# Kernel optimization log

Measured on AMD Instinct MI355X. Metric: run time of the kernel, lower is better.

## Reference

```python
import jax, jax.numpy as jnp
import numpy as np

EPS_BN = 1e-5
EPS_NORM = 1e-12


def setup_inputs() -> dict:
    dim, mid, k = 128, 32, 3
    b, h, w = 8, 128, 128
    key = jax.random.key(0)
    ks = jax.random.split(key, 16)
    s = 0.05
    return {
        "x": jax.random.normal(ks[0], (b, dim, h, w), jnp.float32),
        "w_spatial_in": jax.random.normal(ks[1], (dim, dim), jnp.float32) * s,
        "w_dw_spatial": jax.random.normal(ks[2], (dim, 1, k), jnp.float32) * s,
        "w_spatial_out": jax.random.normal(ks[3], (dim, dim), jnp.float32) * s,
        "w_ch_in": jax.random.normal(ks[4], (dim, dim), jnp.float32) * s,
        "w_ch_dw": jax.random.normal(ks[5], (dim, 1, k), jnp.float32) * s,
        "w_ch_out": jax.random.normal(ks[6], (dim, dim), jnp.float32) * s,
        "w_mlp1": jax.random.normal(ks[7], (mid, dim), jnp.float32) * s,
        "b_mlp1": jax.random.normal(ks[8], (mid,), jnp.float32) * s,
        "w_mlp2": jax.random.normal(ks[9], (dim, mid), jnp.float32) * s,
        "b_mlp2": jax.random.normal(ks[10], (dim,), jnp.float32) * s,
        "diff_weight": jnp.float32(1.0),
        "bn_gamma": jnp.ones((dim,), jnp.float32),
        "bn_beta": jnp.zeros((dim,), jnp.float32),
        "w_out_proj": jax.random.normal(ks[11], (dim, dim), jnp.float32) * s,
    }


def _dwconv1d(seq, wk):
    # seq: [b, c, L], wk: [c, 1, k] depthwise, 'same' padding
    c = seq.shape[1]
    k = wk.shape[-1]
    return jax.lax.conv_general_dilated(
        seq, wk, window_strides=(1,), padding=[(k // 2, k // 2)],
        dimension_numbers=("NCH", "OIH", "NCH"), feature_group_count=c)


def _ocs_forward(x, w_spatial_in, w_dw_spatial, w_spatial_out,
                 w_ch_in, w_ch_dw, w_ch_out,
                 w_mlp1, b_mlp1, w_mlp2, b_mlp2,
                 diff_weight, bn_gamma, bn_beta, w_out_proj):
    b, c, h, w = x.shape
    L = h * w
    alpha = beta = eta = 1.0

    # ---- scan indices (4 orders) ----
    idx_row = jnp.arange(L)
    gy, gx = jnp.meshgrid(jnp.arange(h), jnp.arange(w), indexing="ij")
    idx_col = (gx * h + gy).reshape(-1)
    orders = [idx_row, idx_row[::-1], idx_col, idx_col[::-1]]

    x_seq0 = x.reshape(b, c, L).transpose(0, 2, 1)  # [b, L, c]

    def scan(idx):
        s = x_seq0[:, idx]                                   # gather   [b,L,c]
        s = jnp.einsum("blc,oc->blo", s, w_spatial_in)       # linear
        s = _dwconv1d(s.transpose(0, 2, 1), w_dw_spatial)    # dw conv  [b,c,L]
        s = jnp.einsum("bcl,oc->blo", s, w_spatial_out)      # linear   [b,L,c]
        s = s.at[:, idx].set(s[:, jnp.arange(L)]) if False else s[:, jnp.argsort(idx)]  # scatter back (inverse perm)
        return s.transpose(0, 2, 1).reshape(b, c, h, w)

    y_sp = (scan(orders[0]) + scan(orders[1]) + scan(orders[2]) + scan(orders[3])) * 0.25

    # ---- channel branch ----
    seq = x.reshape(b, c, L)
    seq = jnp.einsum("oc,bcl->bol", w_ch_in, seq)
    seq = _dwconv1d(seq, w_ch_dw)
    seq = jnp.einsum("oc,bcl->bol", w_ch_out, seq)
    gap = x.mean((2, 3))                                     # [b,c]
    gap = gap / jnp.maximum(jnp.linalg.norm(gap, axis=1, keepdims=True), EPS_NORM)
    m = jnp.einsum("bi,bj->bij", gap, gap)                   # [b,c,c]
    seq_agg = jnp.einsum("bij,bjl->bil", m, seq)             # [b,c,L]
    h1 = jax.nn.silu(jnp.einsum("mc,bcl->bml", w_mlp1, seq_agg) + b_mlp1[None, :, None])
    y_ch = (jnp.einsum("cm,bml->bcl", w_mlp2, h1) + b_mlp2[None, :, None]).reshape(b, c, h, w)

    # ---- difference branch (reflect-pad 4-neighbor abs diff) ----
    p = jnp.pad(x, ((0, 0), (0, 0), (1, 1), (1, 1)), mode="reflect")
    cx = p[:, :, 1:-1, 1:-1]
    diff = (jnp.abs(cx - p[:, :, 1:-1, :-2]) + jnp.abs(cx - p[:, :, 1:-1, 2:])
            + jnp.abs(cx - p[:, :, :-2, 1:-1]) + jnp.abs(cx - p[:, :, 2:, 1:-1])) * 0.25
    y_diff = x + diff_weight * diff

    # ---- combine, 1x1 proj, batchnorm (training-mode batch stats) ----
    y = alpha * y_sp + beta * y_ch + eta * y_diff
    y = jnp.einsum("oc,bchw->bohw", w_out_proj, y)
    mu = y.mean((0, 2, 3))
    var = y.var((0, 2, 3))
    y = (y - mu[None, :, None, None]) * jax.lax.rsqrt(var + EPS_BN)[None, :, None, None]
    y = y * bn_gamma[None, :, None, None] + bn_beta[None, :, None, None]
    return y


def reference(x, w_spatial_in, w_dw_spatial, w_spatial_out, w_ch_in, w_ch_dw,
              w_ch_out, w_mlp1, b_mlp1, w_mlp2, b_mlp2, diff_weight,
              bn_gamma, bn_beta, w_out_proj):
    return _ocs_forward(x, w_spatial_in, w_dw_spatial, w_spatial_out,
                        w_ch_in, w_ch_dw, w_ch_out, w_mlp1, b_mlp1,
                        w_mlp2, b_mlp2, diff_weight, bn_gamma, bn_beta,
                        w_out_proj)
```

## Files before the change

### kernel.cpp

```cpp
#include <hip/hip_runtime.h>
#include <hip/hip_bf16.h>

#define C 128
#define L 16384
#define B 8
#define MID 32
#define NBL (B * L)

typedef unsigned short ushort_t;
typedef __attribute__((ext_vector_type(8))) short s8v;
typedef __attribute__((ext_vector_type(4))) float f4v;

__device__ __forceinline__ unsigned short f2bf(float f) {
    union { float f; unsigned int u; } a; a.f = f;
    unsigned int u = a.u;
    return (unsigned short)((u + 0x7fffu + ((u >> 16) & 1u)) >> 16);
}

__device__ __forceinline__ void load8(const ushort_t* p, float* f) {
    uint4 u = *(const uint4*)p;
    f[0] = __uint_as_float(u.x << 16); f[1] = __uint_as_float(u.x & 0xffff0000u);
    f[2] = __uint_as_float(u.y << 16); f[3] = __uint_as_float(u.y & 0xffff0000u);
    f[4] = __uint_as_float(u.z << 16); f[5] = __uint_as_float(u.z & 0xffff0000u);
    f[6] = __uint_as_float(u.w << 16); f[7] = __uint_as_float(u.w & 0xffff0000u);
}

__device__ __forceinline__ void zero8(float* f) {
#pragma unroll
    for (int j = 0; j < 8; j++) f[j] = 0.f;
}

__device__ __forceinline__ void store8(ushort_t* p, const float* f) {
    union { ushort_t h[8]; uint4 q; } u;
#pragma unroll
    for (int j = 0; j < 8; j++) u.h[j] = f2bf(f[j]);
    *(uint4*)p = u.q;
}

__device__ __forceinline__ void ld8f(const float* p, float* f) {
    float4 a = *(const float4*)p;
    float4 b = *(const float4*)(p + 4);
    f[0] = a.x; f[1] = a.y; f[2] = a.z; f[3] = a.w;
    f[4] = b.x; f[5] = b.y; f[6] = b.z; f[7] = b.w;
}

__global__ __launch_bounds__(256) void k_cvt(const float* __restrict__ x,
                                             ushort_t* __restrict__ xb,
                                             float* __restrict__ gap) {
    __shared__ float xs[64][129];
    const int bid = blockIdx.x;
    const int b = bid >> 8;
    const int l0 = (bid & 255) * 64;
    const int tid = threadIdx.x;
    const int c = tid >> 1, h = tid & 1;
    const float* src = x + ((size_t)(b * C + c)) * L + l0 + h * 32;
    float s = 0.f;
#pragma unroll
    for (int j = 0; j < 8; j++) {
        float4 v = *(const float4*)(src + j * 4);
        s += (v.x + v.y) + (v.z + v.w);
        int lb = h * 32 + j * 4;
        xs[lb + 0][c] = v.x; xs[lb + 1][c] = v.y;
        xs[lb + 2][c] = v.z; xs[lb + 3][c] = v.w;
    }
    s += __shfl_xor(s, 1);
    if (h == 0) atomicAdd(&gap[b * C + c], s);
    __syncthreads();
    const int l = tid & 63, quarter = tid >> 6, cb = quarter * 32;
    union { ushort_t hh[32]; uint4 q[4]; } u;
#pragma unroll
    for (int k = 0; k < 32; k++) u.hh[k] = f2bf(xs[l][cb + k]);
    uint4* dst = (uint4*)(xb + ((size_t)(b * L + l0 + l)) * C + cb);
#pragma unroll
    for (int k = 0; k < 4; k++) dst[k] = u.q[k];
}

__global__ __launch_bounds__(128) void k_prep_b(const float* __restrict__ gap,
                                                const float* __restrict__ w1,
                                                const float* __restrict__ Wco,
                                                float* __restrict__ a,
                                                float* __restrict__ gw) {
    int b = blockIdx.x, c = threadIdx.x;
    __shared__ float gl[C];
    __shared__ float red[C];
    float v = gap[b * C + c] * (1.f / (float)L);
    red[c] = v * v;
    __syncthreads();
    for (int w = 64; w > 0; w >>= 1) {
        if (c < w) red[c] += red[c + w];
        __syncthreads();
    }
    float nrm = fmaxf(sqrtf(red[0]), 1e-12f);
    float gc = v / nrm;
    gl[c] = gc;
    __syncthreads();
    if (c < MID) {
        float s = 0.f;
        for (int k = 0; k < C; k++) s = fmaf(w1[c * C + k], gl[k], s);
        a[b * MID + c] = s;
    }
    {
        float s = 0.f;
        for (int k = 0; k < C; k++) s = fmaf(gl[k], Wco[k * C + c], s);
        gw[b * C + c] = s;
    }
}

__global__ __launch_bounds__(128) void k_prep_w(const float* __restrict__ Win,
                                                const float* __restrict__ Wci,
                                                const float* __restrict__ Wproj,
                                                const float* __restrict__ Wout,
                                                const float* __restrict__ w2,
                                                const float* __restrict__ b2,
                                                const float* __restrict__ wds,
                                                const float* __restrict__ wcd,
                                                ushort_t* __restrict__ Wio,
                                                ushort_t* __restrict__ Wcat,
                                                float* __restrict__ bp,
                                                float* __restrict__ kwS,
                                                float* __restrict__ kw1,
                                                float* __restrict__ kd0,
                                                float* __restrict__ kd1,
                                                float* __restrict__ kd2) {
    int o = blockIdx.x, c = threadIdx.x;
    __shared__ float pr[C];
    pr[c] = Wproj[o * C + c];
    __syncthreads();
    Wio[o * C + c] = f2bf(Win[o * C + c]);
    Wio[(C + o) * C + c] = f2bf(Wci[o * C + c]);
    float s = 0.f;
    for (int k = 0; k < C; k++) s = fmaf(pr[k], Wout[k * C + c], s);
    Wcat[o * 288 + c] = f2bf(s);
    Wcat[o * 288 + 128 + c] = f2bf(pr[c]);
    if (c < MID) {
        float s2 = 0.f;
        for (int k = 0; k < C; k++) s2 = fmaf(pr[k], w2[k * MID + c], s2);
        Wcat[o * 288 + 256 + c] = f2bf(s2);
    }
    if (c == 0) {
        float s3 = 0.f;
        for (int k = 0; k < C; k++) s3 = fmaf(pr[k], b2[k], s3);
        bp[o] = s3;
    }
    if (o == 0) {
        kwS[c] = 0.25f * (wds[3 * c] + wds[3 * c + 2]);
        kw1[c] = wds[3 * c + 1];
        kd0[c] = wcd[3 * c];
        kd1[c] = wcd[3 * c + 1];
        kd2[c] = wcd[3 * c + 2];
    }
}

__global__ __launch_bounds__(512, 1) void k_gemm1(const ushort_t* __restrict__ xb,
                                                  const ushort_t* __restrict__ Wio,
                                                  ushort_t* __restrict__ tu) {
    __shared__ ushort_t wl[128 * 136];
    const int tid = threadIdx.x;
    const int bid = blockIdx.x;
    const int b = bid >> 8;
    const int ms = (bid >> 7) & 1;
    const int lt = bid & 127;
    {
        int row = tid >> 2, qq = tid & 3;
        const uint4* s4 = (const uint4*)(Wio + (ms * C + row) * C + qq * 32);
        uint4* d4 = (uint4*)(wl + row * 136 + qq * 32);
        d4[0] = s4[0]; d4[1] = s4[1]; d4[2] = s4[2]; d4[3] = s4[3];
    }
    __syncthreads();
    const int wave = tid >> 6, lane = tid & 63;
    const int l0 = lt * 128 + wave * 16;
    const int n = lane & 15, q = lane >> 4;
    const ushort_t* brow = xb + ((size_t)(b * L + l0 + n)) * C + q * 8;
    s8v bfrag[4];
#pragma unroll
    for (int ks = 0; ks < 4; ks++) bfrag[ks] = *(const s8v*)(brow + ks * 32);
    f4v acc[8];
#pragma unroll
    for (int i = 0; i < 8; i++) acc[i] = (f4v){0.f, 0.f, 0.f, 0.f};
#pragma unroll
    for (int ks = 0; ks < 4; ks++) {
#pragma unroll
        for (int mt = 0; mt < 8; mt++) {
            s8v af = *(const s8v*)(wl + (mt * 16 + n) * 136 + ks * 32 + q * 8);
            acc[mt] = __builtin_amdgcn_mfma_f32_16x16x32_bf16(af, bfrag[ks], acc[mt], 0, 0, 0);
        }
    }
    ushort_t* orow = tu + ((size_t)(b * L + l0 + n)) * 256 + ms * C + q * 4;
#pragma unroll
    for (int mt = 0; mt < 8; mt++) {
        union { ushort_t h[4]; uint2 q2; } u;
#pragma unroll
        for (int i = 0; i < 4; i++) u.h[i] = f2bf(acc[mt][i]);
        *(uint2*)(orow + mt * 16) = u.q2;
    }
}

__global__ __launch_bounds__(256) void k_mid(const ushort_t* __restrict__ tu,
                                             const ushort_t* __restrict__ xb,
                                             const float* __restrict__ kwS,
                                             const float* __restrict__ kw1,
                                             const float* __restrict__ kd0,
                                             const float* __restrict__ kd1,
                                             const float* __restrict__ kd2,
                                             const float* __restrict__ gw,
                                             const float* __restrict__ a,
                                             const float* __restrict__ b1,
                                             const float* __restrict__ pdw,
                                             ushort_t* __restrict__ Kb) {
    const int tid = threadIdx.x;
    const int cc = tid & 15, p = tid >> 4;
    const int bid = blockIdx.x;
    const int b = bid >> 10;
    const int l = (bid & 1023) * 16 + p;
    const int y = l >> 7, xg = l & 127;
    const int c0 = cc * 8;
    const size_t rb = (size_t)b * L;

    const int rL = (l > 0) ? (l - 1) : -1;
    const int rR = (l < L - 1) ? (l + 1) : -1;
    const int rU = (y > 0) ? (l - 128) : ((xg > 0) ? (16256 + xg - 1) : -1);
    const int rD = (y < 127) ? (l + 128) : ((xg < 127) ? (xg + 1) : -1);
    const int sL = (xg > 0) ? (l - 1) : (l + 1);
    const int sR = (xg < 127) ? (l + 1) : (l - 1);
    const int sU = (y > 0) ? (l - 128) : (l + 128);
    const int sD = (y < 127) ? (l + 128) : (l - 128);

    float tC[8], tLe[8], tRi[8], tUp[8], tDo[8];
    load8(tu + (rb + l) * 256 + c0, tC);
    if (rL >= 0) load8(tu + (rb + rL) * 256 + c0, tLe); else zero8(tLe);
    if (rR >= 0) load8(tu + (rb + rR) * 256 + c0, tRi); else zero8(tRi);
    if (rU >= 0) load8(tu + (rb + rU) * 256 + c0, tUp); else zero8(tUp);
    if (rD >= 0) load8(tu + (rb + rD) * 256 + c0, tDo); else zero8(tDo);

    float uC[8], uL8[8], uR8[8];
    load8(tu + (rb + l) * 256 + 128 + c0, uC);
    if (rL >= 0) load8(tu + (rb + rL) * 256 + 128 + c0, uL8); else zero8(uL8);
    if (rR >= 0) load8(tu + (rb + rR) * 256 + 128 + c0, uR8); else zero8(uR8);

    float xC[8], xL8[8], xR8[8], xU8[8], xD8[8];
    load8(xb + (rb + l) * C + c0, xC);
    load8(xb + (rb + sL) * C + c0, xL8);
    load8(xb + (rb + sR) * C + c0, xR8);
    load8(xb + (rb + sU) * C + c0, xU8);
    load8(xb + (rb + sD) * C + c0, xD8);

    float kS[8], k1[8], d0[8], d1[8], d2[8], gv[8];
    ld8f(kwS + c0, kS); ld8f(kw1 + c0, k1);
    ld8f(kd0 + c0, d0); ld8f(kd1 + c0, d1); ld8f(kd2 + c0, d2);
    ld8f(gw + b * C + c0, gv);
    const float dwt = pdw[0] * 0.25f;

    float ct[8], yd[8];
    float s1 = 0.f;
#pragma unroll
    for (int j = 0; j < 8; j++) {
        ct[j] = kS[j] * ((tLe[j] + tRi[j]) + (tUp[j] + tDo[j])) + k1[j] * tC[j];
        float vv = d0[j] * uL8[j] + d1[j] * uC[j] + d2[j] * uR8[j];
        s1 = fmaf(gv[j], vv, s1);
        float cen = xC[j];
        float d = fabsf(cen - xL8[j]) + fabsf(cen - xR8[j]) +
                  fabsf(cen - xU8[j]) + fabsf(cen - xD8[j]);
        yd[j] = fmaf(dwt, d, cen);
    }
    s1 += __shfl_xor(s1, 1);
    s1 += __shfl_xor(s1, 2);
    s1 += __shfl_xor(s1, 4);
    s1 += __shfl_xor(s1, 8);

    ushort_t* kr = Kb + (rb + l) * 288;
    store8(kr + c0, ct);
    store8(kr + 128 + c0, yd);
    if (cc < 4) {
        float av[8], bv[8], sv[8];
        ld8f(a + b * MID + cc * 8, av);
        ld8f(b1 + cc * 8, bv);
#pragma unroll
        for (int j = 0; j < 8; j++) {
            float pre = fmaf(av[j], s1, bv[j]);
            sv[j] = pre / (1.f + __expf(-pre));
        }
        store8(kr + 256 + cc * 8, sv);
    }
}

__global__ __launch_bounds__(512, 1) void k_gemm2(const ushort_t* __restrict__ Kb,
                                                  const ushort_t* __restrict__ Wcat,
                                                  const float* __restrict__ bp,
                                                  float* __restrict__ outp) {
    __shared__ ushort_t wl[64 * 296];
    const int tid = threadIdx.x;
    const int bid = blockIdx.x;
    const int b = bid >> 8;
    const int ms = (bid >> 7) & 1;
    const int lt = bid & 127;
    for (int i = 0; i < 5; i++) {
        int idx = tid + i * 512;
        if (idx < 2304) {
            int row = idx / 36, col = idx - row * 36;
            *(uint4*)(wl + row * 296 + col * 8) =
                *(const uint4*)(Wcat + (ms * 64 + row) * 288 + col * 8);
        }
    }
    __syncthreads();
    const int wave = tid >> 6, lane = tid & 63;
    const int l0 = lt * 128 + wave * 16;
    const int n = lane & 15, q = lane >> 4;
    const ushort_t* brow = Kb + ((size_t)(b * L + l0 + n)) * 288 + q * 8;
    f4v acc[4];
#pragma unroll
    for (int i = 0; i < 4; i++) acc[i] = (f4v){0.f, 0.f, 0.f, 0.f};
#pragma unroll
    for (int ks = 0; ks < 9; ks++) {
        s8v bf_ = *(const s8v*)(brow + ks * 32);
#pragma unroll
        for (int mt = 0; mt < 4; mt++) {
            s8v af = *(const s8v*)(wl + (mt * 16 + n) * 296 + ks * 32 + q * 8);
            acc[mt] = __builtin_amdgcn_mfma_f32_16x16x32_bf16(af, bf_, acc[mt], 0, 0, 0);
        }
    }
#pragma unroll
    for (int mt = 0; mt < 4; mt++) {
        int o0 = ms * 64 + mt * 16 + q * 4;
        float4 bv = *(const float4*)(bp + o0);
        float ba[4] = {bv.x, bv.y, bv.z, bv.w};
#pragma unroll
        for (int i = 0; i < 4; i++) {
            outp[((size_t)(b * C + o0 + i)) * L + l0 + n] = acc[mt][i] + ba[i];
        }
    }
}

__global__ __launch_bounds__(256) void k_bnstats2(const float* __restrict__ outp,
                                                  float* __restrict__ stats) {
    const int bo = blockIdx.x;
    const int o = bo & (C - 1);
    const float4* p = (const float4*)(outp + (size_t)bo * L);
    float s = 0.f, sq = 0.f;
    for (int i = threadIdx.x; i < L / 4; i += 256) {
        float4 v = p[i];
        s += (v.x + v.y) + (v.z + v.w);
        sq += v.x * v.x + v.y * v.y + v.z * v.z + v.w * v.w;
    }
    __shared__ float rs[256], rq[256];
    rs[threadIdx.x] = s; rq[threadIdx.x] = sq;
    __syncthreads();
    for (int w = 128; w > 0; w >>= 1) {
        if (threadIdx.x < w) {
            rs[threadIdx.x] += rs[threadIdx.x + w];
            rq[threadIdx.x] += rq[threadIdx.x + w];
        }
        __syncthreads();
    }
    if (threadIdx.x == 0) {
        atomicAdd(&stats[o], rs[0]);
        atomicAdd(&stats[C + o], rq[0]);
    }
}

__global__ void k_bnfin(const float* __restrict__ stats, const float* __restrict__ gamma,
                        const float* __restrict__ beta, float* __restrict__ scsh) {
    int o = threadIdx.x;
    float n = (float)NBL;
    float mu = stats[o] / n;
    float var = stats[C + o] / n - mu * mu;
    float sc = gamma[o] * rsqrtf(var + 1e-5f);
    scsh[o] = sc;
    scsh[C + o] = fmaf(-mu, sc, beta[o]);
}

__global__ __launch_bounds__(256) void k_bnapply(float* __restrict__ outp,
                                                 const float* __restrict__ scsh) {
    int bo = blockIdx.x;
    int o = bo & (C - 1);
    float sc = scsh[o], sh = scsh[C + o];
    float4* p = (float4*)(outp + (size_t)bo * L);
    for (int i = threadIdx.x; i < L / 4; i += 256) {
        float4 v = p[i];
        v.x = fmaf(v.x, sc, sh);
        v.y = fmaf(v.y, sc, sh);
        v.z = fmaf(v.z, sc, sh);
        v.w = fmaf(v.w, sc, sh);
        p[i] = v;
    }
}

extern "C" void kernel_launch(void* const* d_in, const int* in_sizes, int n_in,
                              void* d_out, int out_size, void* d_ws, size_t ws_size,
                              hipStream_t stream) {
    const float* x = (const float*)d_in[0];
    const float* Win = (const float*)d_in[1];
    const float* wds = (const float*)d_in[2];
    const float* Wout = (const float*)d_in[3];
    const float* Wci = (const float*)d_in[4];
    const float* wcd = (const float*)d_in[5];
    const float* Wco = (const float*)d_in[6];
    const float* w1 = (const float*)d_in[7];
    const float* b1 = (const float*)d_in[8];
    const float* w2 = (const float*)d_in[9];
    const float* b2 = (const float*)d_in[10];
    const float* pdw = (const float*)d_in[11];
    const float* gamma = (const float*)d_in[12];
    const float* beta = (const float*)d_in[13];
    const float* Wproj = (const float*)d_in[14];

    char* wsb = (char*)d_ws;
    ushort_t* xb = (ushort_t*)wsb;
    ushort_t* tu = (ushort_t*)(wsb + 33554432);
    ushort_t* Kb = (ushort_t*)(wsb + 100663296);
    char* S = wsb + 176160768;
    float* gap  = (float*)(S + 0);
    float* stats= (float*)(S + 4096);
    float* scsh = (float*)(S + 5120);
    float* a    = (float*)(S + 6144);
    float* gw   = (float*)(S + 7168);
    float* bp   = (float*)(S + 11264);
    float* kwS  = (float*)(S + 11776);
    float* kw1  = (float*)(S + 12288);
    float* kd0  = (float*)(S + 12800);
    float* kd1  = (float*)(S + 13312);
    float* kd2  = (float*)(S + 13824);
    ushort_t* Wio  = (ushort_t*)(S + 14336);
    ushort_t* Wcat = (ushort_t*)(S + 79872);
    float* outp = (float*)d_out;

    hipMemsetAsync(S, 0, 5120, stream);
    k_cvt<<<2048, 256, 0, stream>>>(x, xb, gap);
    k_prep_b<<<8, 128, 0, stream>>>(gap, w1, Wco, a, gw);
    k_prep_w<<<128, 128, 0, stream>>>(Win, Wci, Wproj, Wout, w2, b2, wds, wcd,
                                      Wio, Wcat, bp, kwS, kw1, kd0, kd1, kd2);
    k_gemm1<<<2048, 512, 0, stream>>>(xb, Wio, tu);
    k_mid<<<8192, 256, 0, stream>>>(tu, xb, kwS, kw1, kd0, kd1, kd2, gw, a, b1, pdw, Kb);
    k_gemm2<<<2048, 512, 0, stream>>>(Kb, Wcat, bp, outp);
    k_bnstats2<<<1024, 256, 0, stream>>>(outp, stats);
    k_bnfin<<<1, 128, 0, stream>>>(stats, gamma, beta, scsh);
    k_bnapply<<<1024, 256, 0, stream>>>(outp, scsh);
}
```

Measured before the change: 313.9 us.

## Fuse mid stencil, second GEMM and BN stats into one kernel via LDS tile

The stencil/mix kernel now writes its 64-position K tile (bf16, 288 channels) into shared memory instead of a global Kb buffer. The same block then runs the second MFMA GEMM against Wcat, read straight from global, and accumulates per-channel sum and sum-of-squares with shuffles and atomics. This removes the Kb round trip through HBM and the separate stats pass over the output. The trade-off is more atomics, per-wave global loads of the weight fragments, and a heavier block, whose occupancy is set to 4 via launch bounds. bnapply is also split over twice as many blocks.

```diff
diff --git a/kernel.cpp b/kernel.cpp
--- a/kernel.cpp
+++ b/kernel.cpp
@@ -30,7 +30,7 @@
     for (int j = 0; j < 8; j++) f[j] = 0.f;
 }
 
-__device__ __forceinline__ void store8(ushort_t* p, const float* f) {
+__device__ __forceinline__ void store8_lds(ushort_t* p, const float* f) {
     union { ushort_t h[8]; uint4 q; } u;
 #pragma unroll
     for (int j = 0; j < 8; j++) u.h[j] = f2bf(f[j]);
@@ -195,165 +195,143 @@
     }
 }
 
-__global__ __launch_bounds__(256) void k_mid(const ushort_t* __restrict__ tu,
-                                             const ushort_t* __restrict__ xb,
-                                             const float* __restrict__ kwS,
-                                             const float* __restrict__ kw1,
-                                             const float* __restrict__ kd0,
-                                             const float* __restrict__ kd1,
-                                             const float* __restrict__ kd2,
-                                             const float* __restrict__ gw,
-                                             const float* __restrict__ a,
-                                             const float* __restrict__ b1,
-                                             const float* __restrict__ pdw,
-                                             ushort_t* __restrict__ Kb) {
+__global__ __launch_bounds__(256, 4) void k_fuse2(
+    const ushort_t* __restrict__ tu, const ushort_t* __restrict__ xb,
+    const float* __restrict__ kwS, const float* __restrict__ kw1,
+    const float* __restrict__ kd0, const float* __restrict__ kd1,
+    const float* __restrict__ kd2, const float* __restrict__ gw,
+    const float* __restrict__ a, const float* __restrict__ b1,
+    const float* __restrict__ pdw, const ushort_t* __restrict__ Wcat,
+    const float* __restrict__ bp, float* __restrict__ outp,
+    float* __restrict__ stats) {
+    __shared__ ushort_t Kl[64 * 296];
     const int tid = threadIdx.x;
-    const int cc = tid & 15, p = tid >> 4;
     const int bid = blockIdx.x;
-    const int b = bid >> 10;
-    const int l = (bid & 1023) * 16 + p;
-    const int y = l >> 7, xg = l & 127;
+    const int b = bid >> 8;
+    const int l0 = (bid & 255) * 64;
+    const size_t rb = (size_t)b * L;
+    const int cc = tid & 15, p16 = tid >> 4;
     const int c0 = cc * 8;
-    const size_t rb = (size_t)b * L;
-
-    const int rL = (l > 0) ? (l - 1) : -1;
-    const int rR = (l < L - 1) ? (l + 1) : -1;
-    const int rU = (y > 0) ? (l - 128) : ((xg > 0) ? (16256 + xg - 1) : -1);
-    const int rD = (y < 127) ? (l + 128) : ((xg < 127) ? (xg + 1) : -1);
-    const int sL = (xg > 0) ? (l - 1) : (l + 1);
-    const int sR = (xg < 127) ? (l + 1) : (l - 1);
-    const int sU = (y > 0) ? (l - 128) : (l + 128);
-    const int sD = (y < 127) ? (l + 128) : (l - 128);
-
-    float tC[8], tLe[8], tRi[8], tUp[8], tDo[8];
-    load8(tu + (rb + l) * 256 + c0, tC);
-    if (rL >= 0) load8(tu + (rb + rL) * 256 + c0, tLe); else zero8(tLe);
-    if (rR >= 0) load8(tu + (rb + rR) * 256 + c0, tRi); else zero8(tRi);
-    if (rU >= 0) load8(tu + (rb + rU) * 256 + c0, tUp); else zero8(tUp);
-    if (rD >= 0) load8(tu + (rb + rD) * 256 + c0, tDo); else zero8(tDo);
-
-    float uC[8], uL8[8], uR8[8];
-    load8(tu + (rb + l) * 256 + 128 + c0, uC);
-    if (rL >= 0) load8(tu + (rb + rL) * 256 + 128 + c0, uL8); else zero8(uL8);
-    if (rR >= 0) load8(tu + (rb + rR) * 256 + 128 + c0, uR8); else zero8(uR8);
-
-    float xC[8], xL8[8], xR8[8], xU8[8], xD8[8];
-    load8(xb + (rb + l) * C + c0, xC);
-    load8(xb + (rb + sL) * C + c0, xL8);
-    load8(xb + (rb + sR) * C + c0, xR8);
-    load8(xb + (rb + sU) * C + c0, xU8);
-    load8(xb + (rb + sD) * C + c0, xD8);
 
     float kS[8], k1[8], d0[8], d1[8], d2[8], gv[8];
     ld8f(kwS + c0, kS); ld8f(kw1 + c0, k1);
     ld8f(kd0 + c0, d0); ld8f(kd1 + c0, d1); ld8f(kd2 + c0, d2);
     ld8f(gw + b * C + c0, gv);
     const float dwt = pdw[0] * 0.25f;
-
-    float ct[8], yd[8];
-    float s1 = 0.f;
-#pragma unroll
-    for (int j = 0; j < 8; j++) {
-        ct[j] = kS[j] * ((tLe[j] + tRi[j]) + (tUp[j] + tDo[j])) + k1[j] * tC[j];
-        float vv = d0[j] * uL8[j] + d1[j] * uC[j] + d2[j] * uR8[j];
-        s1 = fmaf(gv[j], vv, s1);
-        float cen = xC[j];
-        float d = fabsf(cen - xL8[j]) + fabsf(cen - xR8[j]) +
-                  fabsf(cen - xU8[j]) + fabsf(cen - xD8[j]);
-        yd[j] = fmaf(dwt, d, cen);
-    }
-    s1 += __shfl_xor(s1, 1);
-    s1 += __shfl_xor(s1, 2);
-    s1 += __shfl_xor(s1, 4);
-    s1 += __shfl_xor(s1, 8);
-
-    ushort_t* kr = Kb + (rb + l) * 288;
-    store8(kr + c0, ct);
-    store8(kr + 128 + c0, yd);
-    if (cc < 4) {
-        float av[8], bv[8], sv[8];
-        ld8f(a + b * MID + cc * 8, av);
-        ld8f(b1 + cc * 8, bv);
+    float av[8], bv[8];
+    if (cc < 4) { ld8f(a + b * MID + cc * 8, av); ld8f(b1 + cc * 8, bv); }
+
+    for (int st = 0; st < 4; st++) {
+        const int p = st * 16 + p16;
+        const int l = l0 + p;
+        const int y = l >> 7, xg = l & 127;
+
+        const int rL = (l > 0) ? (l - 1) : -1;
+        const int rR = (l < L - 1) ? (l + 1) : -1;
+        const int rU = (y > 0) ? (l - 128) : ((xg > 0) ? (16256 + xg - 1) : -1);
+        const int rD = (y < 127) ? (l + 128) : ((xg < 127) ? (xg + 1) : -1);
+        const int sL = (xg > 0) ? (l - 1) : (l + 1);
+        const int sR = (xg < 127) ? (l + 1) : (l - 1);
+        const int sU = (y > 0) ? (l - 128) : (l + 128);
+        const int sD = (y < 127) ? (l + 128) : (l - 128);
+
+        float tC[8], tLe[8], tRi[8], tUp[8], tDo[8];
+        load8(tu + (rb + l) * 256 + c0, tC);
+        if (rL >= 0) load8(tu + (rb + rL) * 256 + c0, tLe); else zero8(tLe);
+        if (rR >= 0) load8(tu + (rb + rR) * 256 + c0, tRi); else zero8(tRi);
+        if (rU >= 0) load8(tu + (rb + rU) * 256 + c0, tUp); else zero8(tUp);
+        if (rD >= 0) load8(tu + (rb + rD) * 256 + c0, tDo); else zero8(tDo);
+
+        float uC[8], uL8[8], uR8[8];
+        load8(tu + (rb + l) * 256 + 128 + c0, uC);
+        if (rL >= 0) load8(tu + (rb + rL) * 256 + 128 + c0, uL8); else zero8(uL8);
+        if (rR >= 0) load8(tu + (rb + rR) * 256 + 128 + c0, uR8); else zero8(uR8);
+
+        float xC[8], xL8[8], xR8[8], xU8[8], xD8[8];
+        load8(xb + (rb + l) * C + c0, xC);
+        load8(xb + (rb + sL) * C + c0, xL8);
+        load8(xb + (rb + sR) * C + c0, xR8);
+        load8(xb + (rb + sU) * C + c0, xU8);
+        load8(xb + (rb + sD) * C + c0, xD8);
+
+        float ct[8], yd[8];
+        float s1 = 0.f;
 #pragma unroll
         for (int j = 0; j < 8; j++) {
-            float pre = fmaf(av[j], s1, bv[j]);
-            sv[j] = pre / (1.f + __expf(-pre));
+            ct[j] = kS[j] * ((tLe[j] + tRi[j]) + (tUp[j] + tDo[j])) + k1[j] * tC[j];
+            float vv = d0[j] * uL8[j] + d1[j] * uC[j] + d2[j] * uR8[j];
+            s1 = fmaf(gv[j], vv, s1);
+            float cen = xC[j];
+            float d = fabsf(cen - xL8[j]) + fabsf(cen - xR8[j]) +
+                      fabsf(cen - xU8[j]) + fabsf(cen - xD8[j]);
+            yd[j] = fmaf(dwt, d, cen);
         }
-        store8(kr + 256 + cc * 8, sv);
-    }
-}
-
-__global__ __launch_bounds__(512, 1) void k_gemm2(const ushort_t* __restrict__ Kb,
-                                                  const ushort_t* __restrict__ Wcat,
-                                                  const float* __restrict__ bp,
-                                                  float* __restrict__ outp) {
-    __shared__ ushort_t wl[64 * 296];
-    const int tid = threadIdx.x;
-    const int bid = blockIdx.x;
-    const int b = bid >> 8;
-    const int ms = (bid >> 7) & 1;
-    const int lt = bid & 127;
-    for (int i = 0; i < 5; i++) {
-        int idx = tid + i * 512;
-        if (idx < 2304) {
-            int row = idx / 36, col = idx - row * 36;
-            *(uint4*)(wl + row * 296 + col * 8) =
-                *(const uint4*)(Wcat + (ms * 64 + row) * 288 + col * 8);
+        s1 += __shfl_xor(s1, 1);
+        s1 += __shfl_xor(s1, 2);
+        s1 += __shfl_xor(s1, 4);
+        s1 += __shfl_xor(s1, 8);
+
+        ushort_t* kr = Kl + p * 296;
+        store8_lds(kr + c0, ct);
+        store8_lds(kr + 128 + c0, yd);
+        if (cc < 4) {
+            float sv[8];
+#pragma unroll
+            for (int j = 0; j < 8; j++) {
+                float pre = fmaf(av[j], s1, bv[j]);
+                sv[j] = pre / (1.f + __expf(-pre));
+            }
+            store8_lds(kr + 256 + cc * 8, sv);
         }
     }
     __syncthreads();
-    const int wave = tid >> 6, lane = tid & 63;
-    const int l0 = lt * 128 + wave * 16;
+
+    const int w = tid >> 6, lane = tid & 63;
     const int n = lane & 15, q = lane >> 4;
-    const ushort_t* brow = Kb + ((size_t)(b * L + l0 + n)) * 288 + q * 8;
-    f4v acc[4];
-#pragma unroll
-    for (int i = 0; i < 4; i++) acc[i] = (f4v){0.f, 0.f, 0.f, 0.f};
+    f4v acc[2][4];
+#pragma unroll
+    for (int m = 0; m < 2; m++)
+#pragma unroll
+        for (int t = 0; t < 4; t++) acc[m][t] = (f4v){0.f, 0.f, 0.f, 0.f};
+    const ushort_t* A0 = Wcat + ((w * 2 + 0) * 16 + n) * 288 + q * 8;
+    const ushort_t* A1 = Wcat + ((w * 2 + 1) * 16 + n) * 288 + q * 8;
 #pragma unroll
     for (int ks = 0; ks < 9; ks++) {
-        s8v bf_ = *(const s8v*)(brow + ks * 32);
-#pragma unroll
-        for (int mt = 0; mt < 4; mt++) {
-            s8v af = *(const s8v*)(wl + (mt * 16 + n) * 296 + ks * 32 + q * 8);
-            acc[mt] = __builtin_amdgcn_mfma_f32_16x16x32_bf16(af, bf_, acc[mt], 0, 0, 0);
+        s8v a0 = *(const s8v*)(A0 + ks * 32);
+        s8v a1 = *(const s8v*)(A1 + ks * 32);
+#pragma unroll
+        for (int t = 0; t < 4; t++) {
+            s8v bf_ = *(const s8v*)(Kl + (t * 16 + n) * 296 + ks * 32 + q * 8);
+            acc[0][t] = __builtin_amdgcn_mfma_f32_16x16x32_bf16(a0, bf_, acc[0][t], 0, 0, 0);
+            acc[1][t] = __builtin_amdgcn_mfma_f32_16x16x32_bf16(a1, bf_, acc[1][t], 0, 0, 0);
         }
     }
-#pragma unroll
-    for (int mt = 0; mt < 4; mt++) {
-        int o0 = ms * 64 + mt * 16 + q * 4;
-        float4 bv = *(const float4*)(bp + o0);
-        float ba[4] = {bv.x, bv.y, bv.z, bv.w};
+
+#pragma unroll
+    for (int mtl = 0; mtl < 2; mtl++) {
+        const int o0 = (w * 2 + mtl) * 16 + q * 4;
+        float4 bpv = *(const float4*)(bp + o0);
+        float ba[4] = {bpv.x, bpv.y, bpv.z, bpv.w};
 #pragma unroll
         for (int i = 0; i < 4; i++) {
-            outp[((size_t)(b * C + o0 + i)) * L + l0 + n] = acc[mt][i] + ba[i];
+            const int o = o0 + i;
+            float s = 0.f, sq = 0.f;
+#pragma unroll
+            for (int t = 0; t < 4; t++) {
+                float v = acc[mtl][t][i] + ba[i];
+                outp[((size_t)(b * C + o)) * L + l0 + t * 16 + n] = v;
+                s += v;
+                sq = fmaf(v, v, sq);
+            }
+            s += __shfl_xor(s, 1); s += __shfl_xor(s, 2);
+            s += __shfl_xor(s, 4); s += __shfl_xor(s, 8);
+            sq += __shfl_xor(sq, 1); sq += __shfl_xor(sq, 2);
+            sq += __shfl_xor(sq, 4); sq += __shfl_xor(sq, 8);
+            if (n == 0) {
+                atomicAdd(&stats[o], s);
+                atomicAdd(&stats[C + o], sq);
+            }
         }
-    }
-}
-
-__global__ __launch_bounds__(256) void k_bnstats2(const float* __restrict__ outp,
-                                                  float* __restrict__ stats) {
-    const int bo = blockIdx.x;
-    const int o = bo & (C - 1);
-    const float4* p = (const float4*)(outp + (size_t)bo * L);
-    float s = 0.f, sq = 0.f;
-    for (int i = threadIdx.x; i < L / 4; i += 256) {
-        float4 v = p[i];
-        s += (v.x + v.y) + (v.z + v.w);
-        sq += v.x * v.x + v.y * v.y + v.z * v.z + v.w * v.w;
-    }
-    __shared__ float rs[256], rq[256];
-    rs[threadIdx.x] = s; rq[threadIdx.x] = sq;
-    __syncthreads();
-    for (int w = 128; w > 0; w >>= 1) {
-        if (threadIdx.x < w) {
-            rs[threadIdx.x] += rs[threadIdx.x + w];
-            rq[threadIdx.x] += rq[threadIdx.x + w];
-        }
-        __syncthreads();
-    }
-    if (threadIdx.x == 0) {
-        atomicAdd(&stats[o], rs[0]);
-        atomicAdd(&stats[C + o], rq[0]);
     }
 }
 
@@ -370,11 +348,13 @@
 
 __global__ __launch_bounds__(256) void k_bnapply(float* __restrict__ outp,
                                                  const float* __restrict__ scsh) {
-    int bo = blockIdx.x;
+    int bid = blockIdx.x;
+    int bo = bid >> 1;
+    int half = bid & 1;
     int o = bo & (C - 1);
     float sc = scsh[o], sh = scsh[C + o];
-    float4* p = (float4*)(outp + (size_t)bo * L);
-    for (int i = threadIdx.x; i < L / 4; i += 256) {
+    float4* p = (float4*)(outp + (size_t)bo * L + half * (L / 2));
+    for (int i = threadIdx.x; i < L / 8; i += 256) {
         float4 v = p[i];
         v.x = fmaf(v.x, sc, sh);
         v.y = fmaf(v.y, sc, sh);
@@ -406,8 +386,7 @@
     char* wsb = (char*)d_ws;
     ushort_t* xb = (ushort_t*)wsb;
     ushort_t* tu = (ushort_t*)(wsb + 33554432);
-    ushort_t* Kb = (ushort_t*)(wsb + 100663296);
-    char* S = wsb + 176160768;
+    char* S = wsb + 100663296;
     float* gap  = (float*)(S + 0);
     float* stats= (float*)(S + 4096);
     float* scsh = (float*)(S + 5120);
@@ -429,9 +408,8 @@
     k_prep_w<<<128, 128, 0, stream>>>(Win, Wci, Wproj, Wout, w2, b2, wds, wcd,
                                       Wio, Wcat, bp, kwS, kw1, kd0, kd1, kd2);
     k_gemm1<<<2048, 512, 0, stream>>>(xb, Wio, tu);
-    k_mid<<<8192, 256, 0, stream>>>(tu, xb, kwS, kw1, kd0, kd1, kd2, gw, a, b1, pdw, Kb);
-    k_gemm2<<<2048, 512, 0, stream>>>(Kb, Wcat, bp, outp);
-    k_bnstats2<<<1024, 256, 0, stream>>>(outp, stats);
+    k_fuse2<<<2048, 256, 0, stream>>>(tu, xb, kwS, kw1, kd0, kd1, kd2, gw, a, b1,
+                                      pdw, Wcat, bp, outp, stats);
     k_bnfin<<<1, 128, 0, stream>>>(stats, gamma, beta, scsh);
-    k_bnapply<<<1024, 256, 0, stream>>>(outp, scsh);
-}
+    k_bnapply<<<2048, 256, 0, stream>>>(outp, scsh);
+}
```

New measurement: 533.6 us. 70.0% more time.

## Fuse BN statistics into GEMM2 epilogue and store bf16 intermediate

Applied to the files above, without the earlier changes.

The second GEMM now writes its pre-BN output as bf16 into reused workspace and computes per-block partial sum and sum-of-squares via shuffles and shared memory. A small deterministic reduction kernel replaces the separate stats pass and its atomics, and the apply kernel reads bf16 and writes fp32 output. This removes one full fp32 read pass and halves the intermediate write traffic. The cost is a bf16 rounding of pre-normalization values, which adds precision error.

```diff
diff --git a/kernel.cpp b/kernel.cpp
--- a/kernel.cpp
+++ b/kernel.cpp
@@ -286,8 +286,11 @@
 __global__ __launch_bounds__(512, 1) void k_gemm2(const ushort_t* __restrict__ Kb,
                                                   const ushort_t* __restrict__ Wcat,
                                                   const float* __restrict__ bp,
-                                                  float* __restrict__ outp) {
+                                                  ushort_t* __restrict__ ob,
+                                                  float* __restrict__ stats_p) {
     __shared__ ushort_t wl[64 * 296];
+    __shared__ float rs_[8][64];
+    __shared__ float rq_[8][64];
     const int tid = threadIdx.x;
     const int bid = blockIdx.x;
     const int b = bid >> 8;
@@ -325,36 +328,50 @@
         float ba[4] = {bv.x, bv.y, bv.z, bv.w};
 #pragma unroll
         for (int i = 0; i < 4; i++) {
-            outp[((size_t)(b * C + o0 + i)) * L + l0 + n] = acc[mt][i] + ba[i];
+            float v = acc[mt][i] + ba[i];
+            ob[((size_t)(b * C + o0 + i)) * L + l0 + n] = f2bf(v);
+            float s = v, sq = v * v;
+            s += __shfl_xor(s, 1); s += __shfl_xor(s, 2);
+            s += __shfl_xor(s, 4); s += __shfl_xor(s, 8);
+            sq += __shfl_xor(sq, 1); sq += __shfl_xor(sq, 2);
+            sq += __shfl_xor(sq, 4); sq += __shfl_xor(sq, 8);
+            if (n == 0) {
+                int ol = mt * 16 + q * 4 + i;
+                rs_[wave][ol] = s;
+                rq_[wave][ol] = sq;
+            }
         }
     }
-}
-
-__global__ __launch_bounds__(256) void k_bnstats2(const float* __restrict__ outp,
-                                                  float* __restrict__ stats) {
-    const int bo = blockIdx.x;
-    const int o = bo & (C - 1);
-    const float4* p = (const float4*)(outp + (size_t)bo * L);
-    float s = 0.f, sq = 0.f;
-    for (int i = threadIdx.x; i < L / 4; i += 256) {
-        float4 v = p[i];
-        s += (v.x + v.y) + (v.z + v.w);
-        sq += v.x * v.x + v.y * v.y + v.z * v.z + v.w * v.w;
-    }
-    __shared__ float rs[256], rq[256];
-    rs[threadIdx.x] = s; rq[threadIdx.x] = sq;
+    __syncthreads();
+    if (tid < 64) {
+        float s = 0.f, sq = 0.f;
+#pragma unroll
+        for (int w = 0; w < 8; w++) { s += rs_[w][tid]; sq += rq_[w][tid]; }
+        stats_p[(size_t)bid * 128 + tid] = s;
+        stats_p[(size_t)bid * 128 + 64 + tid] = sq;
+    }
+}
+
+__global__ __launch_bounds__(256) void k_bnred(const float* __restrict__ stats_p,
+                                               float* __restrict__ stats) {
+    const int j = blockIdx.x;
+    const int stat = j >> 7, o = j & 127;
+    const int ms = o >> 6, ol = o & 63;
+    const int tid = threadIdx.x;
+    float s = 0.f;
+    for (int idx = tid; idx < 1024; idx += 256) {
+        int b = idx >> 7, lt = idx & 127;
+        int bid = b * 256 + ms * 128 + lt;
+        s += stats_p[(size_t)bid * 128 + stat * 64 + ol];
+    }
+    __shared__ float red[256];
+    red[tid] = s;
     __syncthreads();
     for (int w = 128; w > 0; w >>= 1) {
-        if (threadIdx.x < w) {
-            rs[threadIdx.x] += rs[threadIdx.x + w];
-            rq[threadIdx.x] += rq[threadIdx.x + w];
-        }
+        if (tid < w) red[tid] += red[tid + w];
         __syncthreads();
     }
-    if (threadIdx.x == 0) {
-        atomicAdd(&stats[o], rs[0]);
-        atomicAdd(&stats[C + o], rq[0]);
-    }
+    if (tid == 0) stats[stat * 128 + o] = red[0];
 }
 
 __global__ void k_bnfin(const float* __restrict__ stats, const float* __restrict__ gamma,
@@ -368,19 +385,26 @@
     scsh[C + o] = fmaf(-mu, sc, beta[o]);
 }
 
-__global__ __launch_bounds__(256) void k_bnapply(float* __restrict__ outp,
+__global__ __launch_bounds__(256) void k_bnapply(const ushort_t* __restrict__ ob,
+                                                 float* __restrict__ outp,
                                                  const float* __restrict__ scsh) {
-    int bo = blockIdx.x;
-    int o = bo & (C - 1);
-    float sc = scsh[o], sh = scsh[C + o];
-    float4* p = (float4*)(outp + (size_t)bo * L);
-    for (int i = threadIdx.x; i < L / 4; i += 256) {
-        float4 v = p[i];
-        v.x = fmaf(v.x, sc, sh);
-        v.y = fmaf(v.y, sc, sh);
-        v.z = fmaf(v.z, sc, sh);
-        v.w = fmaf(v.w, sc, sh);
-        p[i] = v;
+    const int bid = blockIdx.x;
+    const int bo = bid >> 1;
+    const int half = bid & 1;
+    const int o = bo & (C - 1);
+    const float sc = scsh[o], sh = scsh[C + o];
+    const ushort_t* src = ob + (size_t)bo * L + half * (L / 2);
+    float* dst = outp + (size_t)bo * L + half * (L / 2);
+    for (int i = threadIdx.x; i < (L / 2) / 8; i += 256) {
+        float f[8];
+        load8(src + i * 8, f);
+        float4 v0, v1;
+        v0.x = fmaf(f[0], sc, sh); v0.y = fmaf(f[1], sc, sh);
+        v0.z = fmaf(f[2], sc, sh); v0.w = fmaf(f[3], sc, sh);
+        v1.x = fmaf(f[4], sc, sh); v1.y = fmaf(f[5], sc, sh);
+        v1.z = fmaf(f[6], sc, sh); v1.w = fmaf(f[7], sc, sh);
+        *(float4*)(dst + i * 8) = v0;
+        *(float4*)(dst + i * 8 + 4) = v1;
     }
 }
 
@@ -405,6 +429,7 @@
 
     char* wsb = (char*)d_ws;
     ushort_t* xb = (ushort_t*)wsb;
+    ushort_t* ob = (ushort_t*)wsb;
     ushort_t* tu = (ushort_t*)(wsb + 33554432);
     ushort_t* Kb = (ushort_t*)(wsb + 100663296);
     char* S = wsb + 176160768;
@@ -421,17 +446,18 @@
     float* kd2  = (float*)(S + 13824);
     ushort_t* Wio  = (ushort_t*)(S + 14336);
     ushort_t* Wcat = (ushort_t*)(S + 79872);
+    float* stats_p = (float*)(S + 155648);
     float* outp = (float*)d_out;
 
-    hipMemsetAsync(S, 0, 5120, stream);
+    hipMemsetAsync(S, 0, 4096, stream);
     k_cvt<<<2048, 256, 0, stream>>>(x, xb, gap);
     k_prep_b<<<8, 128, 0, stream>>>(gap, w1, Wco, a, gw);
     k_prep_w<<<128, 128, 0, stream>>>(Win, Wci, Wproj, Wout, w2, b2, wds, wcd,
                                       Wio, Wcat, bp, kwS, kw1, kd0, kd1, kd2);
     k_gemm1<<<2048, 512, 0, stream>>>(xb, Wio, tu);
     k_mid<<<8192, 256, 0, stream>>>(tu, xb, kwS, kw1, kd0, kd1, kd2, gw, a, b1, pdw, Kb);
-    k_gemm2<<<2048, 512, 0, stream>>>(Kb, Wcat, bp, outp);
-    k_bnstats2<<<1024, 256, 0, stream>>>(outp, stats);
+    k_gemm2<<<2048, 512, 0, stream>>>(Kb, Wcat, bp, ob, stats_p);
+    k_bnred<<<256, 256, 0, stream>>>(stats_p, stats);
     k_bnfin<<<1, 128, 0, stream>>>(stats, gamma, beta, scsh);
-    k_bnapply<<<1024, 256, 0, stream>>>(outp, scsh);
-}
+    k_bnapply<<<2048, 256, 0, stream>>>(ob, outp, scsh);
+}
```

Measured after the change: 315.1 us. No clear change (+0.4%).
